# Optimization experiments

Hardware: AMD Instinct MI355X
Metric: run time of the kernel (lower is better)

Reference implementation:

```python
import jax, jax.numpy as jnp
import numpy as np

WINDOW_SIZE = 11
SIGMA = 1.5
C1 = 0.01 ** 2
C2 = 0.03 ** 2


def _gaussian_1d(window_size, sigma):
    x = np.arange(window_size, dtype=np.float32)
    g = np.exp(-((x - window_size // 2) ** 2) / (2.0 * sigma ** 2))
    g = g / g.sum()
    return jnp.asarray(g, dtype=jnp.float32)


def _blur(x, g1d):
    # Separable depthwise Gaussian blur, SAME padding.
    # x: [B, C, H, W]; mathematically identical to conv with outer(g, g).
    c = x.shape[1]
    pad = WINDOW_SIZE // 2
    kh = jnp.broadcast_to(g1d.reshape(1, 1, WINDOW_SIZE, 1), (c, 1, WINDOW_SIZE, 1))
    kw = jnp.broadcast_to(g1d.reshape(1, 1, 1, WINDOW_SIZE), (c, 1, 1, WINDOW_SIZE))
    dn = ('NCHW', 'OIHW', 'NCHW')
    x = jax.lax.conv_general_dilated(x, kh, (1, 1), [(pad, pad), (0, 0)],
                                     dimension_numbers=dn, feature_group_count=c)
    x = jax.lax.conv_general_dilated(x, kw, (1, 1), [(0, 0), (pad, pad)],
                                     dimension_numbers=dn, feature_group_count=c)
    return x


def setup_inputs() -> dict:
    key = jax.random.key(0)
    k1, k2 = jax.random.split(key)
    shape = (32, 1, 512, 512)
    img1 = jax.random.uniform(k1, shape, dtype=jnp.float32)
    img2 = jax.random.uniform(k2, shape, dtype=jnp.float32)
    return {"img1": img1, "img2": img2}


def reference(img1, img2):
    g1d = _gaussian_1d(WINDOW_SIZE, SIGMA)
    mu1 = _blur(img1, g1d)
    mu2 = _blur(img2, g1d)
    mu1_sq = mu1 * mu1
    mu2_sq = mu2 * mu2
    mu1_mu2 = mu1 * mu2
    sigma1_sq = _blur(img1 * img1, g1d) - mu1_sq
    sigma2_sq = _blur(img2 * img2, g1d) - mu2_sq
    sigma12 = _blur(img1 * img2, g1d) - mu1_mu2
    ssim_map = ((2.0 * mu1_mu2 + C1) * (2.0 * sigma12 + C2)) / (
        (mu1_sq + mu2_sq + C1) * (sigma1_sq + sigma2_sq + C2))
    return ssim_map.mean()  # size_average=True
```

## Files before the change

kernel.cpp:

```cpp
#include <hip/hip_runtime.h>

#define HH 512
#define WW 512
#define BATCH 32
#define BH 16
#define NB (HH / BH)
#define TPB 256
#define VTW 528
#define NBLOCKS (NB * BATCH)
#define CBASE 0xAAAAAAAAu

__global__ __launch_bounds__(TPB) void ssim_main(
    const float* __restrict__ img1,
    const float* __restrict__ img2,
    unsigned* __restrict__ counter,
    float* __restrict__ partial,
    float* __restrict__ out)
{
  constexpr float G[11] = {
      0.00102838f, 0.00759876f, 0.03600077f, 0.10936070f, 0.21300553f,
      0.26601171f,
      0.21300553f, 0.10936070f, 0.03600077f, 0.00759876f, 0.00102838f};
  constexpr float C1 = 1.0e-4f;
  constexpr float C2 = 9.0e-4f;

  const int tid  = threadIdx.x;
  const int band = blockIdx.x;
  const int bat  = blockIdx.y;
  const int r0   = band * BH;
  const float* p1 = img1 + (size_t)bat * (HH * WW);
  const float* p2 = img2 + (size_t)bat * (HH * WW);
  const int c0 = tid * 2;

  __shared__ __align__(16) float hs[2][2][5][VTW];
  __shared__ float  wsum[4];
  __shared__ double dsum[4];
  __shared__ int    amlast;

  if (tid < 16) {
    const int p = tid >> 3, o = tid & 7;
#pragma unroll
    for (int r = 0; r < 2; ++r)
#pragma unroll
      for (int a = 0; a < 5; ++a) {
        hs[p][r][a][o]       = 0.f;
        hs[p][r][a][520 + o] = 0.f;
      }
  }

  float2 w1[12], w2[12];
#pragma unroll
  for (int j = 0; j < 12; ++j) {
    const int r = r0 - 5 + j;
    float2 a = make_float2(0.f, 0.f), b = a;
    if (r >= 0 && r < HH) {
      a = *(const float2*)(p1 + r * WW + c0);
      b = *(const float2*)(p2 + r * WW + c0);
    }
    w1[j] = a; w2[j] = b;
  }

  __syncthreads();

  float ssum = 0.f;

#pragma unroll
  for (int q = 0; q < BH; q += 2) {
    const int pr = (q >> 1) & 1;

    float2 ta1 = make_float2(0.f, 0.f), ta2 = ta1, tb1 = ta1, tb2 = ta1;
    if (q + 2 < BH) {
      const int ra = r0 + 7 + q;
      const int rb = r0 + 8 + q;
      if (ra < HH) {
        ta1 = *(const float2*)(p1 + ra * WW + c0);
        ta2 = *(const float2*)(p2 + ra * WW + c0);
      }
      if (rb < HH) {
        tb1 = *(const float2*)(p1 + rb * WW + c0);
        tb2 = *(const float2*)(p2 + rb * WW + c0);
      }
    }

    float acc[2][5][2];
#pragma unroll
    for (int r = 0; r < 2; ++r)
#pragma unroll
      for (int a = 0; a < 5; ++a) { acc[r][a][0] = 0.f; acc[r][a][1] = 0.f; }

#pragma unroll
    for (int j = 0; j < 12; ++j) {
      const float2 xa = w1[j];
      const float2 ya = w2[j];
      const float xv[2] = {xa.x, xa.y};
      const float yv[2] = {ya.x, ya.y};
#pragma unroll
      for (int i = 0; i < 2; ++i) {
        const float x  = xv[i], y = yv[i];
        const float xx = x * x, yy = y * y, xy = x * y;
        if (j < 11) {
          const float g = G[j];
          acc[0][0][i] = fmaf(g, x,  acc[0][0][i]);
          acc[0][1][i] = fmaf(g, y,  acc[0][1][i]);
          acc[0][2][i] = fmaf(g, xx, acc[0][2][i]);
          acc[0][3][i] = fmaf(g, yy, acc[0][3][i]);
          acc[0][4][i] = fmaf(g, xy, acc[0][4][i]);
        }
        if (j >= 1) {
          const float g = G[j - 1];
          acc[1][0][i] = fmaf(g, x,  acc[1][0][i]);
          acc[1][1][i] = fmaf(g, y,  acc[1][1][i]);
          acc[1][2][i] = fmaf(g, xx, acc[1][2][i]);
          acc[1][3][i] = fmaf(g, yy, acc[1][3][i]);
          acc[1][4][i] = fmaf(g, xy, acc[1][4][i]);
        }
      }
    }

#pragma unroll
    for (int r = 0; r < 2; ++r)
#pragma unroll
      for (int a = 0; a < 5; ++a)
        ((float2*)(&hs[pr][r][a][0]))[4 + tid] =
            make_float2(acc[r][a][0], acc[r][a][1]);

    __syncthreads();

#pragma unroll
    for (int r = 0; r < 2; ++r) {
      float h[5][2];
#pragma unroll
      for (int a = 0; a < 5; ++a) {
        const float2* r2 = (const float2*)(&hs[pr][r][a][0]);
        float x[14];
#pragma unroll
        for (int m = 0; m < 7; ++m) {
          const float2 v = r2[tid + 1 + m];
          x[2 * m]     = v.x;
          x[2 * m + 1] = v.y;
        }
#pragma unroll
        for (int j = 0; j < 2; ++j) {
          float hv = 0.f;
#pragma unroll
          for (int k = 0; k < 11; ++k) hv = fmaf(G[k], x[j + k + 1], hv);
          h[a][j] = hv;
        }
      }

#pragma unroll
      for (int j = 0; j < 2; ++j) {
        const float mu1 = h[0][j], mu2 = h[1][j];
        const float mu12 = mu1 * mu2;
        const float mu1s = mu1 * mu1;
        const float mu2s = mu2 * mu2;
        const float sg1  = h[2][j] - mu1s;
        const float sg2  = h[3][j] - mu2s;
        const float sg12 = h[4][j] - mu12;
        const float num = (2.f * mu12 + C1) * (2.f * sg12 + C2);
        const float den = (mu1s + mu2s + C1) * (sg1 + sg2 + C2);
        float rn = __builtin_amdgcn_rcpf(den);
        rn = rn * fmaf(-den, rn, 2.0f);
        ssum = fmaf(num, rn, ssum);
      }
    }

#pragma unroll
    for (int j = 0; j < 10; ++j) { w1[j] = w1[j + 2]; w2[j] = w2[j + 2]; }
    w1[10] = ta1; w2[10] = ta2;
    w1[11] = tb1; w2[11] = tb2;
  }

#pragma unroll
  for (int off = 32; off > 0; off >>= 1) ssum += __shfl_xor(ssum, off, 64);
  if ((tid & 63) == 0) wsum[tid >> 6] = ssum;
  __syncthreads();
  if (tid == 0) {
    const float bsum = wsum[0] + wsum[1] + wsum[2] + wsum[3];
    atomicExch(&partial[bat * NB + band], bsum);
    __threadfence();
    const unsigned old = atomicAdd(counter, 1u);
    amlast = (old == CBASE + (unsigned)NBLOCKS - 1u) ? 1 : 0;
  }
  __syncthreads();
  if (amlast) {
    double s = 0.0;
#pragma unroll
    for (int i = tid; i < NBLOCKS; i += TPB)
      s += (double)atomicAdd(&partial[i], 0.0f);
#pragma unroll
    for (int off = 32; off > 0; off >>= 1) s += __shfl_xor(s, off, 64);
    if ((tid & 63) == 0) dsum[tid >> 6] = s;
    __syncthreads();
    if (tid == 0)
      out[0] = (float)((dsum[0] + dsum[1] + dsum[2] + dsum[3]) /
                       (double)((size_t)BATCH * HH * WW));
  }
}

extern "C" void kernel_launch(void* const* d_in, const int* in_sizes, int n_in,
                              void* d_out, int out_size, void* d_ws, size_t ws_size,
                              hipStream_t stream) {
  const float* img1 = (const float*)d_in[0];
  const float* img2 = (const float*)d_in[1];
  float* out = (float*)d_out;
  unsigned* counter = (unsigned*)d_ws;
  float* partial = (float*)((char*)d_ws + 16);
  dim3 grid(NB, BATCH);
  ssim_main<<<grid, TPB, 0, stream>>>(img1, img2, counter, partial, out);
}
```

Baseline: 141.1 us.

## Remap horizontal pass to one row per half-block with float4 reads, single LDS buffer

The horizontal blur pass now assigns each half of the block to one of the two output rows, so each thread computes four adjacent columns from five float4 LDS reads per quantity instead of two rows of two columns each. The double-buffered LDS staging becomes a single buffer with an extra barrier per iteration. The outer row loop is no longer unrolled and launch bounds ask for four blocks per CU, aiming to cut register and LDS pressure and raise occupancy. The extra barrier and the rolled loop add synchronisation and loop overhead.

```diff
diff --git a/kernel.cpp b/kernel.cpp
--- a/kernel.cpp
+++ b/kernel.cpp
@@ -10,7 +10,8 @@
 #define NBLOCKS (NB * BATCH)
 #define CBASE 0xAAAAAAAAu
 
-__global__ __launch_bounds__(TPB) void ssim_main(
+
+__global__ __launch_bounds__(TPB, 4) void ssim_main(
     const float* __restrict__ img1,
     const float* __restrict__ img2,
     unsigned* __restrict__ counter,
@@ -31,8 +32,10 @@
   const float* p1 = img1 + (size_t)bat * (HH * WW);
   const float* p2 = img2 + (size_t)bat * (HH * WW);
   const int c0 = tid * 2;
-
-  __shared__ __align__(16) float hs[2][2][5][VTW];
+  const int rr = tid >> 7;
+  const int cg = tid & 127;
+
+  __shared__ __align__(16) float pb[2][5][VTW];
   __shared__ float  wsum[4];
   __shared__ double dsum[4];
   __shared__ int    amlast;
@@ -40,12 +43,10 @@
   if (tid < 16) {
     const int p = tid >> 3, o = tid & 7;
 #pragma unroll
-    for (int r = 0; r < 2; ++r)
-#pragma unroll
-      for (int a = 0; a < 5; ++a) {
-        hs[p][r][a][o]       = 0.f;
-        hs[p][r][a][520 + o] = 0.f;
-      }
+    for (int a = 0; a < 5; ++a) {
+      pb[p][a][o]       = 0.f;
+      pb[p][a][520 + o] = 0.f;
+    }
   }
 
   float2 w1[12], w2[12];
@@ -64,10 +65,8 @@
 
   float ssum = 0.f;
 
-#pragma unroll
+#pragma unroll 1
   for (int q = 0; q < BH; q += 2) {
-    const int pr = (q >> 1) & 1;
-
     float2 ta1 = make_float2(0.f, 0.f), ta2 = ta1, tb1 = ta1, tb2 = ta1;
     if (q + 2 < BH) {
       const int ra = r0 + 7 + q;
@@ -99,20 +98,20 @@
         const float x  = xv[i], y = yv[i];
         const float xx = x * x, yy = y * y, xy = x * y;
         if (j < 11) {
-          const float g = G[j];
-          acc[0][0][i] = fmaf(g, x,  acc[0][0][i]);
-          acc[0][1][i] = fmaf(g, y,  acc[0][1][i]);
-          acc[0][2][i] = fmaf(g, xx, acc[0][2][i]);
-          acc[0][3][i] = fmaf(g, yy, acc[0][3][i]);
-          acc[0][4][i] = fmaf(g, xy, acc[0][4][i]);
+          const float gk = G[j];
+          acc[0][0][i] = fmaf(gk, x,  acc[0][0][i]);
+          acc[0][1][i] = fmaf(gk, y,  acc[0][1][i]);
+          acc[0][2][i] = fmaf(gk, xx, acc[0][2][i]);
+          acc[0][3][i] = fmaf(gk, yy, acc[0][3][i]);
+          acc[0][4][i] = fmaf(gk, xy, acc[0][4][i]);
         }
         if (j >= 1) {
-          const float g = G[j - 1];
-          acc[1][0][i] = fmaf(g, x,  acc[1][0][i]);
-          acc[1][1][i] = fmaf(g, y,  acc[1][1][i]);
-          acc[1][2][i] = fmaf(g, xx, acc[1][2][i]);
-          acc[1][3][i] = fmaf(g, yy, acc[1][3][i]);
-          acc[1][4][i] = fmaf(g, xy, acc[1][4][i]);
+          const float gk = G[j - 1];
+          acc[1][0][i] = fmaf(gk, x,  acc[1][0][i]);
+          acc[1][1][i] = fmaf(gk, y,  acc[1][1][i]);
+          acc[1][2][i] = fmaf(gk, xx, acc[1][2][i]);
+          acc[1][3][i] = fmaf(gk, yy, acc[1][3][i]);
+          acc[1][4][i] = fmaf(gk, xy, acc[1][4][i]);
         }
       }
     }
@@ -121,49 +120,49 @@
     for (int r = 0; r < 2; ++r)
 #pragma unroll
       for (int a = 0; a < 5; ++a)
-        ((float2*)(&hs[pr][r][a][0]))[4 + tid] =
+        ((float2*)(&pb[r][a][0]))[4 + tid] =
             make_float2(acc[r][a][0], acc[r][a][1]);
 
     __syncthreads();
 
-#pragma unroll
-    for (int r = 0; r < 2; ++r) {
-      float h[5][2];
-#pragma unroll
-      for (int a = 0; a < 5; ++a) {
-        const float2* r2 = (const float2*)(&hs[pr][r][a][0]);
-        float x[14];
-#pragma unroll
-        for (int m = 0; m < 7; ++m) {
-          const float2 v = r2[tid + 1 + m];
-          x[2 * m]     = v.x;
-          x[2 * m + 1] = v.y;
-        }
-#pragma unroll
-        for (int j = 0; j < 2; ++j) {
-          float hv = 0.f;
-#pragma unroll
-          for (int k = 0; k < 11; ++k) hv = fmaf(G[k], x[j + k + 1], hv);
-          h[a][j] = hv;
-        }
-      }
-
-#pragma unroll
-      for (int j = 0; j < 2; ++j) {
-        const float mu1 = h[0][j], mu2 = h[1][j];
-        const float mu12 = mu1 * mu2;
-        const float mu1s = mu1 * mu1;
-        const float mu2s = mu2 * mu2;
-        const float sg1  = h[2][j] - mu1s;
-        const float sg2  = h[3][j] - mu2s;
-        const float sg12 = h[4][j] - mu12;
-        const float num = (2.f * mu12 + C1) * (2.f * sg12 + C2);
-        const float den = (mu1s + mu2s + C1) * (sg1 + sg2 + C2);
-        float rn = __builtin_amdgcn_rcpf(den);
-        rn = rn * fmaf(-den, rn, 2.0f);
-        ssum = fmaf(num, rn, ssum);
-      }
-    }
+    float h[5][4];
+#pragma unroll
+    for (int a = 0; a < 5; ++a) {
+      const float4* r4 = (const float4*)(&pb[rr][a][0]);
+      const float4 X0 = r4[cg];
+      const float4 X1 = r4[cg + 1];
+      const float4 X2 = r4[cg + 2];
+      const float4 X3 = r4[cg + 3];
+      const float4 X4 = r4[cg + 4];
+      const float x[20] = {X0.x, X0.y, X0.z, X0.w, X1.x, X1.y, X1.z, X1.w,
+                           X2.x, X2.y, X2.z, X2.w, X3.x, X3.y, X3.z, X3.w,
+                           X4.x, X4.y, X4.z, X4.w};
+#pragma unroll
+      for (int j = 0; j < 4; ++j) {
+        float hv = 0.f;
+#pragma unroll
+        for (int k = 0; k < 11; ++k) hv = fmaf(G[k], x[j + 3 + k], hv);
+        h[a][j] = hv;
+      }
+    }
+
+#pragma unroll
+    for (int j = 0; j < 4; ++j) {
+      const float mu1 = h[0][j], mu2 = h[1][j];
+      const float mu12 = mu1 * mu2;
+      const float mu1s = mu1 * mu1;
+      const float mu2s = mu2 * mu2;
+      const float sg1  = h[2][j] - mu1s;
+      const float sg2  = h[3][j] - mu2s;
+      const float sg12 = h[4][j] - mu12;
+      const float num = (2.f * mu12 + C1) * (2.f * sg12 + C2);
+      const float den = (mu1s + mu2s + C1) * (sg1 + sg2 + C2);
+      float rn = __builtin_amdgcn_rcpf(den);
+      rn = rn * fmaf(-den, rn, 2.0f);
+      ssum = fmaf(num, rn, ssum);
+    }
+
+    __syncthreads();
 
 #pragma unroll
     for (int j = 0; j < 10; ++j) { w1[j] = w1[j + 2]; w2[j] = w2[j + 2]; }
@@ -185,7 +184,6 @@
   __syncthreads();
   if (amlast) {
     double s = 0.0;
-#pragma unroll
     for (int i = tid; i < NBLOCKS; i += TPB)
       s += (double)atomicAdd(&partial[i], 0.0f);
 #pragma unroll
```

After: 130.3 us. 7.6% less time.
